# Performance work log

Hardware: AMD Instinct MI355X
Metric: run time of the kernel (lower is better)

The kernel has to match this reference:

```python
import jax, jax.numpy as jnp
import numpy as np
from jax import lax

_SQ2 = np.sqrt(2.0)
_H2 = (np.array([[1.0, 1.0], [1.0, -1.0]]) / _SQ2).astype(np.complex64)
_BN_INV = 1.0 / np.sqrt(1.0 + 1e-5)  # eval-mode BN, running_mean=0, running_var=1

# wire 0 is the most-significant bit of the 4-qubit basis index (PennyLane convention)
def _cnot_perm(c, t):
    p = np.arange(16)
    for b in range(16):
        if (b >> (3 - c)) & 1:
            p[b] = b ^ (1 << (3 - t))
    return p

# CNOT(0,1) then CNOT(1,2) then CNOT(2,3) then CNOT(3,0); psi_out = psi_in[perm]
_p01, _p12, _p23, _p30 = _cnot_perm(0, 1), _cnot_perm(1, 2), _cnot_perm(2, 3), _cnot_perm(3, 0)
_PTOT = _p01[_p12[_p23[_p30]]]
# PauliZ expectation signs: (16 basis states, 4 wires)
_ZM = np.array([[1.0 - 2.0 * ((b >> (3 - w)) & 1) for w in range(4)] for b in range(16)], np.float32)


def _make_unitaries(w0, w1):
    """w0, w1: (C,2). Circuit: H^4 -> RY(w0[0],w0[1],w0[0],w0[1]) -> RZ(w1 same pattern) -> CNOT ring."""
    ty = jnp.stack([w0[:, 0], w0[:, 1], w0[:, 0], w0[:, 1]], axis=1)  # (C,4)
    tz = jnp.stack([w1[:, 0], w1[:, 1], w1[:, 0], w1[:, 1]], axis=1)
    c, s = jnp.cos(ty / 2), jnp.sin(ty / 2)
    ry = jnp.stack([jnp.stack([c, -s], -1), jnp.stack([s, c], -1)], -2).astype(jnp.complex64)  # (C,4,2,2)
    ph = jnp.exp(-0.5j * tz.astype(jnp.complex64))  # (C,4)
    zr = jnp.zeros_like(ph)
    rz = jnp.stack([jnp.stack([ph, zr], -1), jnp.stack([zr, jnp.conj(ph)], -1)], -2)  # (C,4,2,2)
    g = rz @ ry @ jnp.asarray(_H2)  # per-wire single-qubit gate, (C,4,2,2)
    U = g[:, 0]
    for w in range(1, 4):  # kron over wires 0..3
        d = U.shape[1]
        U = jnp.einsum('cij,ckl->cikjl', U, g[:, w]).reshape(U.shape[0], d * 2, d * 2)
    return U[:, _PTOT, :]  # fold the CNOT-ring permutation into U


def _conv_bn_relu(x, w, g, b):
    y = lax.conv_general_dilated(x, w, (1, 1), ((1, 1), (1, 1)),
                                 dimension_numbers=('NCHW', 'OIHW', 'NCHW'))
    y = y * (g * _BN_INV)[None, :, None, None] + b[None, :, None, None]
    return jax.nn.relu(y)


def _bn_relu(x, g, b):
    return jax.nn.relu(x * (g * _BN_INV)[None, :, None, None] + b[None, :, None, None])


def _maxpool2(x):
    return lax.reduce_window(x, -jnp.inf, lax.max, (1, 1, 2, 2), (1, 1, 2, 2), 'VALID')


def _quantum_stage(e4, q_w0, q_w1):
    B, C, H, W = e4.shape
    xp = jnp.pad(e4, ((0, 0), (0, 0), (1, 2), (1, 2)))  # F.pad(1,2,1,2)
    # 4x4 patches, stride 1, row-major (matches torch unfold->view ordering): (B,C,H,W,16)
    patches = jnp.stack([xp[:, :, i:i + H, j:j + W] for i in range(4) for j in range(4)], axis=-1)
    nrm = jnp.sqrt(jnp.sum(patches * patches, axis=-1, keepdims=True))
    psi0 = (patches / jnp.maximum(nrm, 1e-12)).astype(jnp.complex64)  # AmplitudeEmbedding(normalize=True)
    U = _make_unitaries(q_w0, q_w1)  # (C,16,16) complex
    psi = jnp.einsum('cij,bchwj->bchwi', U, psi0)
    probs = psi.real ** 2 + psi.imag ** 2
    ev = jnp.einsum('bchwi,iq->bchwq', probs, jnp.asarray(_ZM))  # <Z_w> per wire
    return (ev.mean(-1) + 1.0) / 2.0


def setup_inputs() -> dict:
    key = jax.random.key(0)
    ks = jax.random.split(key, 18)
    conv_w = lambda k, o, i: jax.random.normal(k, (o, i, 3, 3), jnp.float32) / np.sqrt(i * 9)
    gamma = lambda k, c: jax.random.uniform(k, (c,), jnp.float32, 0.75, 1.25)
    beta = lambda k, c: 0.1 * jax.random.normal(k, (c,), jnp.float32)
    return {
        'x': jax.random.normal(ks[0], (8, 1, 256, 256), jnp.float32),
        'w1': conv_w(ks[1], 32, 1), 'g1': gamma(ks[2], 32), 'b1': beta(ks[3], 32),
        'w2': conv_w(ks[4], 64, 32), 'g2': gamma(ks[5], 64), 'b2': beta(ks[6], 64),
        'w3': conv_w(ks[7], 128, 64), 'g3': gamma(ks[8], 128), 'b3': beta(ks[9], 128),
        'w4': conv_w(ks[10], 256, 128), 'g4': gamma(ks[11], 256), 'b4': beta(ks[12], 256),
        'q_w0': 0.5 * jax.random.normal(ks[13], (256, 2), jnp.float32),
        'q_w1': 0.5 * jax.random.normal(ks[14], (256, 2), jnp.float32),
        'g5': gamma(ks[15], 256), 'b5': beta(ks[16], 256),
    }


def reference(x, w1, g1, b1, w2, g2, b2, w3, g3, b3, w4, g4, b4, q_w0, q_w1, g5, b5):
    e1 = _conv_bn_relu(x, w1, g1, b1)                 # (8,32,256,256)
    e2 = _conv_bn_relu(_maxpool2(e1), w2, g2, b2)     # (8,64,128,128)
    e3 = _conv_bn_relu(_maxpool2(e2), w3, g3, b3)     # (8,128,64,64)
    e4 = _conv_bn_relu(_maxpool2(e3), w4, g4, b4)     # (8,256,32,32)
    q = _quantum_stage(e4, q_w0, q_w1)                # (8,256,32,32)
    out4 = _bn_relu(q, g5, b5)
    return (e1, e2, e3, out4)
```

## Files before the change

### kernel.cpp

```cpp
#include <hip/hip_runtime.h>
#include <cstdint>
#include <cstddef>

#define BN_INV 0.9999950000374997f

typedef __attribute__((ext_vector_type(8))) _Float16 h8v;
typedef __attribute__((ext_vector_type(4))) float f4v;
typedef __attribute__((ext_vector_type(2))) float f2v;

__device__ __forceinline__ void fsplit(float v, ushort& h, ushort& l) {
    _Float16 hh = (_Float16)v;
    _Float16 ll = (_Float16)(v - (float)hh);
    h = __builtin_bit_cast(ushort, hh);
    l = __builtin_bit_cast(ushort, ll);
}

__device__ __forceinline__ void repack_one(
    const float* __restrict__ w, ushort* __restrict__ dst, int CIN, int i)
{
    int ocf = i / (CIN * 9);
    int r = i % (CIN * 9);
    int ic = r / 9;
    int tap = r % 9;
    int ocg = ocf >> 6, oc = ocf & 63;
    int chunk = ic >> 5, q = (ic >> 3) & 3, j = ic & 7;
    int nch = CIN >> 5;
    ushort h, l;
    fsplit(w[i], h, l);
    size_t base = (size_t)((ocg * nch + chunk) * 2) * 18432
                + (size_t)tap * 2048 + q * 512 + oc * 8 + j;
    dst[base] = h;
    dst[base + 18432] = l;
}

__global__ __launch_bounds__(256) void prep_conv1_kernel(
    const float* __restrict__ w0, const float* __restrict__ w1,
    float* __restrict__ U,
    const float* __restrict__ w2, ushort* __restrict__ wb2,
    const float* __restrict__ w3, ushort* __restrict__ wb3,
    const float* __restrict__ w4, ushort* __restrict__ wb4,
    const float* __restrict__ x, const float* __restrict__ wt,
    const float* __restrict__ g, const float* __restrict__ be,
    float* __restrict__ out, ushort* __restrict__ pooled)
{
    __shared__ float s_in[4][132];

    int blk = blockIdx.x;
    int tid = threadIdx.x;

    if (blk >= 2048) {
        if (blk >= 2424)     { repack_one(w4, wb4, 128, (blk - 2424) * 256 + tid); return; }
        if (blk >= 2136)     { repack_one(w3, wb3,  64, (blk - 2136) * 256 + tid); return; }
        if (blk >= 2064)     { repack_one(w2, wb2,  32, (blk - 2064) * 256 + tid); return; }

        int idx = (blk - 2048) * 256 + tid;
        int c = idx >> 4, r = idx & 15;
        float gr[4][2][2], gi[4][2][2];
        const float inv_sq2 = 0.70710678118654752f;
#pragma unroll
        for (int w = 0; w < 4; ++w) {
            float ty = w0[c * 2 + (w & 1)];
            float tz = w1[c * 2 + (w & 1)];
            float cy = cosf(0.5f * ty), sy = sinf(0.5f * ty);
            float cz = cosf(0.5f * tz), sz = sinf(0.5f * tz);
            float r00 = (cy - sy) * inv_sq2, r01 = (cy + sy) * inv_sq2;
            float r10 = (cy + sy) * inv_sq2, r11 = (sy - cy) * inv_sq2;
            gr[w][0][0] = cz * r00; gi[w][0][0] = -sz * r00;
            gr[w][0][1] = cz * r01; gi[w][0][1] = -sz * r01;
            gr[w][1][0] = cz * r10; gi[w][1][0] =  sz * r10;
            gr[w][1][1] = cz * r11; gi[w][1][1] =  sz * r11;
        }
        const int PTOT[16] = {0,13,3,14,6,11,5,8,12,1,15,2,10,7,9,4};
        int rp = PTOT[r];
        float* Uo = U + (size_t)c * 512 + r * 32;
#pragma unroll
        for (int cc = 0; cc < 16; ++cc) {
            float pr = 1.f, pi = 0.f;
#pragma unroll
            for (int w = 0; w < 4; ++w) {
                int ib = (rp >> (3 - w)) & 1, jb = (cc >> (3 - w)) & 1;
                float ar = gr[w][ib][jb], ai = gi[w][ib][jb];
                float nr = pr * ar - pi * ai;
                float ni = pr * ai + pi * ar;
                pr = nr; pi = ni;
            }
            Uo[cc * 2 + 0] = pr;
            Uo[cc * 2 + 1] = pi;
        }
        return;
    }

    int b = blk >> 8;
    int rest = blk & 255;
    int ty0 = (rest >> 1) * 2;
    int tx0 = (rest & 1) * 128;

    for (int i = tid; i < 520; i += 256) {
        int yy = i / 130, xx = i % 130;
        int gy = ty0 + yy - 1, gx = tx0 + xx - 1;
        float v = 0.f;
        if (gy >= 0 && gy < 256 && gx >= 0 && gx < 256)
            v = x[(size_t)b * 65536 + gy * 256 + gx];
        s_in[yy][xx] = v;
    }
    __syncthreads();

    int xx = ((tid >> 2) << 1) | (tid & 1);
    int yy = (tid >> 1) & 1;
    float t[3][3];
#pragma unroll
    for (int i = 0; i < 3; ++i)
#pragma unroll
        for (int j = 0; j < 3; ++j) t[i][j] = s_in[yy + i][xx + j];

    bool wr_pool = (tid & 3) == 0;
    ushort* op = pooled + (((size_t)b * 128 + (ty0 >> 1)) * 128 + (tx0 >> 1) + (tid >> 2)) * 64;

    size_t obase = ((size_t)b * 32) * 65536 + (size_t)(ty0 + yy) * 256 + (tx0 + xx);
#pragma unroll
    for (int k = 0; k < 4; ++k) {
        uint4 uh, ul;
#pragma unroll
        for (int j = 0; j < 8; ++j) {
            const int oc = k * 8 + j;
            float s = wt[oc*9+0] * t[0][0] + wt[oc*9+1] * t[0][1] + wt[oc*9+2] * t[0][2]
                    + wt[oc*9+3] * t[1][0] + wt[oc*9+4] * t[1][1] + wt[oc*9+5] * t[1][2]
                    + wt[oc*9+6] * t[2][0] + wt[oc*9+7] * t[2][1] + wt[oc*9+8] * t[2][2];
            s = s * (g[oc] * BN_INV) + be[oc];
            s = fmaxf(s, 0.f);
            out[obase + (size_t)oc * 65536] = s;
            float p = fmaxf(s, __shfl_xor(s, 1));
            p = fmaxf(p, __shfl_xor(p, 2));
            ushort h, l;
            fsplit(p, h, l);
            uint hw = (uint)h, lw = (uint)l;
            if (j == 0) { uh.x = hw; ul.x = lw; }
            else if (j == 1) { uh.x |= hw << 16; ul.x |= lw << 16; }
            else if (j == 2) { uh.y = hw; ul.y = lw; }
            else if (j == 3) { uh.y |= hw << 16; ul.y |= lw << 16; }
            else if (j == 4) { uh.z = hw; ul.z = lw; }
            else if (j == 5) { uh.z |= hw << 16; ul.z |= lw << 16; }
            else if (j == 6) { uh.w = hw; ul.w = lw; }
            else             { uh.w |= hw << 16; ul.w |= lw << 16; }
        }
        if (wr_pool) {
            *(uint4*)(op + 8 * k) = uh;
            *(uint4*)(op + 32 + 8 * k) = ul;
        }
    }
}

template <int CIN, int COUT, int HW, bool POOL>
__global__ __launch_bounds__(512) void conv3x3_mfma_split(
    const ushort* __restrict__ in,
    const ushort* __restrict__ wb,
    const float* __restrict__ g, const float* __restrict__ be,
    float* __restrict__ out,
    ushort* __restrict__ pooled)
{
    constexpr int NCH = CIN / 32;
    constexpr int NTX = HW / 16;
    constexpr int NT = NTX * (HW / 8);
    constexpr int NOCG = COUT / 64;
    constexpr int PS = 72;
    constexpr int BUFSZ = 180 * PS;
    constexpr int NBUF = (NCH > 1) ? 2 : 1;

    __shared__ __align__(16) ushort s_in[NBUF * BUFSZ];

    constexpr int NWG = NT * NOCG * 8;
    int bid = blockIdx.x;
    bid = (bid & 7) * (NWG >> 3) + (bid >> 3);

    int tile = bid % NT;
    int rest = bid / NT;
    int ocg = rest % NOCG;
    int b = rest / NOCG;
    int x0 = (tile % NTX) * 16;
    int y0 = (tile / NTX) * 8;

    int tid = threadIdx.x;
    int wv = tid >> 6;
    int lane = tid & 63;
    int n = lane & 15;
    int q = lane >> 4;
    int oc_half = (wv & 1) * 32;
    int sg = wv >> 1;

    int ib[2];
#pragma unroll
    for (int f = 0; f < 2; ++f)
        ib[f] = ((sg * 2 + f) * 18 + n) * PS + q * 8;
    int iwa0 = q * 512 + (oc_half + n) * 8;
    int iwa1 = q * 512 + (oc_half + 16 + n) * 8;

    const ushort* inb = in + (size_t)b * HW * HW * 2 * CIN;

    f4v acc[2][2];
#pragma unroll
    for (int a = 0; a < 2; ++a)
#pragma unroll
        for (int f = 0; f < 2; ++f) acc[a][f] = (f4v){0.f, 0.f, 0.f, 0.f};

    auto stage = [&](int ch, int bsel) {
#pragma unroll
        for (int it = 0; it < 6; ++it) {
            int i = tid + it * 512;
            if (i < 2880) {
                int pos = i >> 4;
                int r2 = i & 15;
                int comp = r2 >> 3;
                int u = r2 & 7;
                int py = pos / 18, px = pos % 18;
                int gy = y0 - 1 + py, gx = x0 - 1 + px;
                uint2 v; v.x = 0u; v.y = 0u;
                if (gy >= 0 && gy < HW && gx >= 0 && gx < HW)
                    v = *(const uint2*)(inb + ((size_t)gy * HW + gx) * (2 * CIN)
                                        + comp * CIN + ch * 32 + u * 4);
                *(uint2*)(&s_in[bsel * BUFSZ + pos * PS + comp * 32 + u * 4]) = v;
            }
        }
    };

    stage(0, 0);
    int cur = 0;
    for (int ch = 0; ch < NCH; ++ch) {
        __syncthreads();
        if (ch + 1 < NCH) stage(ch + 1, cur ^ 1);

        const ushort* wc = wb + (size_t)((ocg * NCH + ch) * 2) * 18432;
        const ushort* sb = &s_in[cur * BUFSZ];
        __builtin_amdgcn_s_setprio(1);
#pragma unroll 3
        for (int tap = 0; tap < 9; ++tap) {
            const int toff = ((tap / 3) * 18 + (tap % 3)) * PS;
            const ushort* wt_ = wc + tap * 2048;
            h8v ah0 = *(const h8v*)(wt_ + iwa0);
            h8v ah1 = *(const h8v*)(wt_ + iwa1);
            h8v al0 = *(const h8v*)(wt_ + 18432 + iwa0);
            h8v al1 = *(const h8v*)(wt_ + 18432 + iwa1);
            h8v bh[2], bl[2];
#pragma unroll
            for (int f = 0; f < 2; ++f) {
                bh[f] = *(const h8v*)(&sb[toff + ib[f]]);
                bl[f] = *(const h8v*)(&sb[toff + ib[f] + 32]);
            }
#pragma unroll
            for (int f = 0; f < 2; ++f) {
                acc[0][f] = __builtin_amdgcn_mfma_f32_16x16x32_f16(ah0, bh[f], acc[0][f], 0, 0, 0);
                acc[1][f] = __builtin_amdgcn_mfma_f32_16x16x32_f16(ah1, bh[f], acc[1][f], 0, 0, 0);
            }
#pragma unroll
            for (int f = 0; f < 2; ++f) {
                acc[0][f] = __builtin_amdgcn_mfma_f32_16x16x32_f16(ah0, bl[f], acc[0][f], 0, 0, 0);
                acc[1][f] = __builtin_amdgcn_mfma_f32_16x16x32_f16(ah1, bl[f], acc[1][f], 0, 0, 0);
            }
#pragma unroll
            for (int f = 0; f < 2; ++f) {
                acc[0][f] = __builtin_amdgcn_mfma_f32_16x16x32_f16(al0, bh[f], acc[0][f], 0, 0, 0);
                acc[1][f] = __builtin_amdgcn_mfma_f32_16x16x32_f16(al1, bh[f], acc[1][f], 0, 0, 0);
            }
        }
        __builtin_amdgcn_s_setprio(0);
        cur ^= (NBUF - 1);
    }

    float vr[2][2][4];
#pragma unroll
    for (int tf = 0; tf < 2; ++tf)
#pragma unroll
        for (int f = 0; f < 2; ++f) {
            int y = y0 + sg * 2 + f;
#pragma unroll
            for (int r = 0; r < 4; ++r) {
                int oc = ocg * 64 + oc_half + tf * 16 + q * 4 + r;
                float v = fmaxf(acc[tf][f][r] * (g[oc] * BN_INV) + be[oc], 0.f);
                vr[tf][f][r] = v;
                out[((size_t)(b * COUT + oc) * HW + y) * HW + (x0 + n)] = v;
            }
        }

    if (POOL) {
#pragma unroll
        for (int tf = 0; tf < 2; ++tf) {
            ushort h[4], l[4];
#pragma unroll
            for (int r = 0; r < 4; ++r) {
                float p = fmaxf(vr[tf][0][r], vr[tf][1][r]);
                p = fmaxf(p, __shfl_xor(p, 1));
                fsplit(p, h[r], l[r]);
            }
            if ((n & 1) == 0) {
                int pyp = (y0 >> 1) + sg;
                int pxp = (x0 + n) >> 1;
                int ocb = ocg * 64 + oc_half + tf * 16 + q * 4;
                ushort* op = pooled
                    + (((size_t)b * (HW / 2) + pyp) * (HW / 2) + pxp) * (2 * COUT);
                uint2 uh, ul;
                uh.x = (uint)h[0] | ((uint)h[1] << 16);
                uh.y = (uint)h[2] | ((uint)h[3] << 16);
                ul.x = (uint)l[0] | ((uint)l[1] << 16);
                ul.y = (uint)l[2] | ((uint)l[3] << 16);
                *(uint2*)(op + ocb) = uh;
                *(uint2*)(op + COUT + ocb) = ul;
            }
        }
    }
}

__global__ __launch_bounds__(256) void quantum_bn_relu(
    const float* __restrict__ e4,
    const float* __restrict__ U,
    const float* __restrict__ g5, const float* __restrict__ b5,
    float* __restrict__ out)
{
    int blk = blockIdx.x;
    int c = blk & 255;
    __shared__ float sp[35][36];
    __shared__ __align__(16) float sU[512];

    int tid = threadIdx.x;
    for (int i = tid; i < 35 * 36; i += 256) ((float*)sp)[i] = 0.f;
    const float4* Usrc = (const float4*)(U + (size_t)c * 512);
    if (tid < 128) ((float4*)sU)[tid] = Usrc[tid];
    float4 pv = ((const float4*)(e4 + (size_t)blk * 1024))[tid];
    __syncthreads();
    {
        int y = tid >> 3, x4 = (tid & 7) << 2;
        sp[y + 1][x4 + 1] = pv.x;
        sp[y + 1][x4 + 2] = pv.y;
        sp[y + 1][x4 + 3] = pv.z;
        sp[y + 1][x4 + 4] = pv.w;
    }
    __syncthreads();

    int y = tid >> 3, x4 = (tid & 7) << 2;
    float rows[4][8];
#pragma unroll
    for (int i = 0; i < 4; ++i) {
        float4 a = *(const float4*)&sp[y + i][x4];
        float4 bq = *(const float4*)&sp[y + i][x4 + 4];
        rows[i][0] = a.x;  rows[i][1] = a.y;  rows[i][2] = a.z;  rows[i][3] = a.w;
        rows[i][4] = bq.x; rows[i][5] = bq.y; rows[i][6] = bq.z; rows[i][7] = bq.w;
    }

    float inv2[4];
#pragma unroll
    for (int k = 0; k < 4; ++k) {
        float ss = 0.f;
#pragma unroll
        for (int i = 0; i < 4; ++i)
#pragma unroll
            for (int j = 0; j < 4; ++j) {
                float v = rows[i][k + j];
                ss += v * v;
            }
        float inv = 1.f / fmaxf(sqrtf(ss), 1e-12f);
        inv2[k] = inv * inv;
    }

    const int   RI[10] = {0, 1, 2, 4, 7, 8, 11, 13, 14, 15};
    const float ZM[10] = {1.f, .5f, .5f, .5f, -.5f, .5f, -.5f, -.5f, -.5f, -1.f};
    const float4* sU4 = (const float4*)sU;

    float s[4] = {0.f, 0.f, 0.f, 0.f};
#pragma unroll
    for (int ii = 0; ii < 10; ++ii) {
        int i = RI[ii];
        f2v p0 = {0.f, 0.f}, p1 = {0.f, 0.f}, p2 = {0.f, 0.f}, p3 = {0.f, 0.f};
#pragma unroll
        for (int jj = 0; jj < 8; ++jj) {
            float4 u = sU4[i * 8 + jj];
            f2v u01 = {u.x, u.y};
            f2v u23 = {u.z, u.w};
            const int e0 = 2 * jj, e1 = 2 * jj + 1;
            p0 += u01 * rows[e0 >> 2][0 + (e0 & 3)];
            p1 += u01 * rows[e0 >> 2][1 + (e0 & 3)];
            p2 += u01 * rows[e0 >> 2][2 + (e0 & 3)];
            p3 += u01 * rows[e0 >> 2][3 + (e0 & 3)];
            p0 += u23 * rows[e1 >> 2][0 + (e1 & 3)];
            p1 += u23 * rows[e1 >> 2][1 + (e1 & 3)];
            p2 += u23 * rows[e1 >> 2][2 + (e1 & 3)];
            p3 += u23 * rows[e1 >> 2][3 + (e1 & 3)];
        }
        float zm = ZM[ii];
        s[0] += (p0.x * p0.x + p0.y * p0.y) * zm;
        s[1] += (p1.x * p1.x + p1.y * p1.y) * zm;
        s[2] += (p2.x * p2.x + p2.y * p2.y) * zm;
        s[3] += (p3.x * p3.x + p3.y * p3.y) * zm;
    }

    float sc = g5[c] * BN_INV, bi = b5[c];
    float4 o;
    o.x = fmaxf(((s[0] * inv2[0] + 1.f) * 0.5f) * sc + bi, 0.f);
    o.y = fmaxf(((s[1] * inv2[1] + 1.f) * 0.5f) * sc + bi, 0.f);
    o.z = fmaxf(((s[2] * inv2[2] + 1.f) * 0.5f) * sc + bi, 0.f);
    o.w = fmaxf(((s[3] * inv2[3] + 1.f) * 0.5f) * sc + bi, 0.f);
    *(float4*)(out + (size_t)blk * 1024 + y * 32 + x4) = o;
}

extern "C" void kernel_launch(void* const* d_in, const int* in_sizes, int n_in,
                              void* d_out, int out_size, void* d_ws, size_t ws_size,
                              hipStream_t stream)
{
    const float* x   = (const float*)d_in[0];
    const float* w1  = (const float*)d_in[1];
    const float* g1  = (const float*)d_in[2];
    const float* b1  = (const float*)d_in[3];
    const float* w2  = (const float*)d_in[4];
    const float* g2  = (const float*)d_in[5];
    const float* b2  = (const float*)d_in[6];
    const float* w3  = (const float*)d_in[7];
    const float* g3  = (const float*)d_in[8];
    const float* b3  = (const float*)d_in[9];
    const float* w4  = (const float*)d_in[10];
    const float* g4  = (const float*)d_in[11];
    const float* b4  = (const float*)d_in[12];
    const float* qw0 = (const float*)d_in[13];
    const float* qw1 = (const float*)d_in[14];
    const float* g5  = (const float*)d_in[15];
    const float* b5  = (const float*)d_in[16];

    float* out = (float*)d_out;
    float* e1  = out;
    float* e2  = out + 16777216;
    float* e3  = out + 25165824;
    float* o4  = out + 29360128;

    float* ws = (float*)d_ws;
    float*  Uw  = ws;
    ushort* wb2 = (ushort*)(ws + 131072);
    ushort* wb3 = (ushort*)(ws + 149504);
    ushort* wb4 = (ushort*)(ws + 223232);
    ushort* pt1 = (ushort*)(ws + 518144);
    ushort* pt2 = (ushort*)(ws + 4712448);
    ushort* pt3 = (ushort*)(ws + 518144);

    prep_conv1_kernel<<<2048 + 1528, 256, 0, stream>>>(
        qw0, qw1, Uw, w2, wb2, w3, wb3, w4, wb4,
        x, w1, g1, b1, e1, pt1);

    conv3x3_mfma_split<32, 64, 128, true><<<1024, 512, 0, stream>>>(pt1, wb2, g2, b2, e2, pt2);

    conv3x3_mfma_split<64, 128, 64, true><<<512, 512, 0, stream>>>(pt2, wb3, g3, b3, e3, pt3);

    conv3x3_mfma_split<128, 256, 32, false><<<256, 512, 0, stream>>>(pt3, wb4, g4, b4, o4, nullptr);

    quantum_bn_relu<<<2048, 256, 0, stream>>>(o4, Uw, g5, b5, o4);
}
```

Measured before the change: 248.2 us.

## Retile conv1 to 4-row blocks with paired outputs; split-stage conv2 input load

The first conv kernel now processes four rows per block, so it launches half as many conv blocks. Each thread computes two adjacent x outputs as float2 vectors, writes them with paired stores, and packs the fp16 hi/lo pool values with cvt_pkrtz. For the single-chunk conv2 case, the input tile is staged in two parts: the rows needed for the first three taps are loaded first, and the remaining loads are issued before those taps run and stored to LDS after them, overlapping global latency with MFMA work. This removes the double-buffer loop for NCH==1, at the cost of an extra barrier and more code paths.

```diff
diff --git a/kernel.cpp b/kernel.cpp
--- a/kernel.cpp
+++ b/kernel.cpp
@@ -43,17 +43,17 @@
     const float* __restrict__ g, const float* __restrict__ be,
     float* __restrict__ out, ushort* __restrict__ pooled)
 {
-    __shared__ float s_in[4][132];
+    __shared__ float s_in[6][132];
 
     int blk = blockIdx.x;
     int tid = threadIdx.x;
 
-    if (blk >= 2048) {
-        if (blk >= 2424)     { repack_one(w4, wb4, 128, (blk - 2424) * 256 + tid); return; }
-        if (blk >= 2136)     { repack_one(w3, wb3,  64, (blk - 2136) * 256 + tid); return; }
-        if (blk >= 2064)     { repack_one(w2, wb2,  32, (blk - 2064) * 256 + tid); return; }
-
-        int idx = (blk - 2048) * 256 + tid;
+    if (blk >= 1024) {
+        if (blk >= 1400)     { repack_one(w4, wb4, 128, (blk - 1400) * 256 + tid); return; }
+        if (blk >= 1112)     { repack_one(w3, wb3,  64, (blk - 1112) * 256 + tid); return; }
+        if (blk >= 1040)     { repack_one(w2, wb2,  32, (blk - 1040) * 256 + tid); return; }
+
+        int idx = (blk - 1024) * 256 + tid;
         int c = idx >> 4, r = idx & 15;
         float gr[4][2][2], gi[4][2][2];
         const float inv_sq2 = 0.70710678118654752f;
@@ -90,12 +90,12 @@
         return;
     }
 
-    int b = blk >> 8;
-    int rest = blk & 255;
-    int ty0 = (rest >> 1) * 2;
+    int b = blk >> 7;
+    int rest = blk & 127;
+    int ty0 = (rest >> 1) * 4;
     int tx0 = (rest & 1) * 128;
 
-    for (int i = tid; i < 520; i += 256) {
+    for (int i = tid; i < 780; i += 256) {
         int yy = i / 130, xx = i % 130;
         int gy = ty0 + yy - 1, gx = tx0 + xx - 1;
         float v = 0.f;
@@ -105,45 +105,66 @@
     }
     __syncthreads();
 
-    int xx = ((tid >> 2) << 1) | (tid & 1);
-    int yy = (tid >> 1) & 1;
-    float t[3][3];
-#pragma unroll
-    for (int i = 0; i < 3; ++i)
-#pragma unroll
-        for (int j = 0; j < 3; ++j) t[i][j] = s_in[yy + i][xx + j];
-
-    bool wr_pool = (tid & 3) == 0;
-    ushort* op = pooled + (((size_t)b * 128 + (ty0 >> 1)) * 128 + (tx0 >> 1) + (tid >> 2)) * 64;
-
-    size_t obase = ((size_t)b * 32) * 65536 + (size_t)(ty0 + yy) * 256 + (tx0 + xx);
+    int w = tid >> 6;
+    int lane = tid & 63;
+    int xp = (w & 1) * 32 + (lane >> 1);
+    int ylo = lane & 1;
+    int y = (w >> 1) * 2 + ylo;
+    int x0s = xp * 2;
+
+    f2v t2[3][3];
+#pragma unroll
+    for (int i = 0; i < 3; ++i) {
+        f2v a = *(const f2v*)&s_in[y + i][x0s];
+        f2v bq = *(const f2v*)&s_in[y + i][x0s + 2];
+        t2[i][0] = a;
+        t2[i][1] = (f2v){a.y, bq.x};
+        t2[i][2] = bq;
+    }
+
+    bool wr_pool = (ylo == 0);
+    int pyp = (ty0 >> 1) + (w >> 1);
+    int pxp = (tx0 >> 1) + xp;
+    ushort* op = pooled + (((size_t)b * 128 + pyp) * 128 + pxp) * 64;
+    size_t obase = ((size_t)b * 32) * 65536 + (size_t)(ty0 + y) * 256 + (tx0 + x0s);
+
 #pragma unroll
     for (int k = 0; k < 4; ++k) {
-        uint4 uh, ul;
-#pragma unroll
-        for (int j = 0; j < 8; ++j) {
-            const int oc = k * 8 + j;
-            float s = wt[oc*9+0] * t[0][0] + wt[oc*9+1] * t[0][1] + wt[oc*9+2] * t[0][2]
-                    + wt[oc*9+3] * t[1][0] + wt[oc*9+4] * t[1][1] + wt[oc*9+5] * t[1][2]
-                    + wt[oc*9+6] * t[2][0] + wt[oc*9+7] * t[2][1] + wt[oc*9+8] * t[2][2];
-            s = s * (g[oc] * BN_INV) + be[oc];
-            s = fmaxf(s, 0.f);
-            out[obase + (size_t)oc * 65536] = s;
-            float p = fmaxf(s, __shfl_xor(s, 1));
-            p = fmaxf(p, __shfl_xor(p, 2));
-            ushort h, l;
-            fsplit(p, h, l);
-            uint hw = (uint)h, lw = (uint)l;
-            if (j == 0) { uh.x = hw; ul.x = lw; }
-            else if (j == 1) { uh.x |= hw << 16; ul.x |= lw << 16; }
-            else if (j == 2) { uh.y = hw; ul.y = lw; }
-            else if (j == 3) { uh.y |= hw << 16; ul.y |= lw << 16; }
-            else if (j == 4) { uh.z = hw; ul.z = lw; }
-            else if (j == 5) { uh.z |= hw << 16; ul.z |= lw << 16; }
-            else if (j == 6) { uh.w = hw; ul.w = lw; }
-            else             { uh.w |= hw << 16; ul.w |= lw << 16; }
+        uint uhw[4], ulw[4];
+#pragma unroll
+        for (int j2 = 0; j2 < 4; ++j2) {
+            const int oc0 = k * 8 + j2 * 2;
+            const int oc1 = oc0 + 1;
+            f2v s0 = {0.f, 0.f}, s1 = {0.f, 0.f};
+#pragma unroll
+            for (int i = 0; i < 3; ++i)
+#pragma unroll
+                for (int j = 0; j < 3; ++j) {
+                    s0 += wt[oc0 * 9 + i * 3 + j] * t2[i][j];
+                    s1 += wt[oc1 * 9 + i * 3 + j] * t2[i][j];
+                }
+            float gs0 = g[oc0] * BN_INV, be0 = be[oc0];
+            float gs1 = g[oc1] * BN_INV, be1 = be[oc1];
+            s0 = s0 * gs0 + (f2v){be0, be0};
+            s1 = s1 * gs1 + (f2v){be1, be1};
+            s0.x = fmaxf(s0.x, 0.f); s0.y = fmaxf(s0.y, 0.f);
+            s1.x = fmaxf(s1.x, 0.f); s1.y = fmaxf(s1.y, 0.f);
+            *(f2v*)(out + obase + (size_t)oc0 * 65536) = s0;
+            *(f2v*)(out + obase + (size_t)oc1 * 65536) = s1;
+            float p0 = fmaxf(s0.x, s0.y);
+            float p1 = fmaxf(s1.x, s1.y);
+            p0 = fmaxf(p0, __shfl_xor(p0, 1));
+            p1 = fmaxf(p1, __shfl_xor(p1, 1));
+            auto hh = __builtin_amdgcn_cvt_pkrtz(p0, p1);
+            uhw[j2] = __builtin_bit_cast(uint, hh);
+            float l0 = p0 - (float)hh.x;
+            float l1 = p1 - (float)hh.y;
+            auto ll = __builtin_amdgcn_cvt_pkrtz(l0, l1);
+            ulw[j2] = __builtin_bit_cast(uint, ll);
         }
         if (wr_pool) {
+            uint4 uh = {uhw[0], uhw[1], uhw[2], uhw[3]};
+            uint4 ul = {ulw[0], ulw[1], ulw[2], ulw[3]};
             *(uint4*)(op + 8 * k) = uh;
             *(uint4*)(op + 32 + 8 * k) = ul;
         }
@@ -202,68 +223,114 @@
 #pragma unroll
         for (int f = 0; f < 2; ++f) acc[a][f] = (f4v){0.f, 0.f, 0.f, 0.f};
 
-    auto stage = [&](int ch, int bsel) {
-#pragma unroll
-        for (int it = 0; it < 6; ++it) {
+    auto elem_addr = [&](int i, int& ldsoff, const ushort*& gsrc) {
+        int pos = i >> 4;
+        int r2 = i & 15;
+        int comp = r2 >> 3;
+        int u = r2 & 7;
+        int py = pos / 18, px = pos % 18;
+        int gy = y0 - 1 + py, gx = x0 - 1 + px;
+        ldsoff = pos * PS + comp * 32 + u * 4;
+        gsrc = (gy >= 0 && gy < HW && gx >= 0 && gx < HW)
+             ? inb + ((size_t)gy * HW + gx) * (2 * CIN) + comp * CIN + u * 4
+             : nullptr;
+    };
+
+#define TAPS(T0, T1)                                                             \
+    _Pragma("unroll")                                                            \
+    for (int tap = T0; tap < T1; ++tap) {                                        \
+        const int toff = ((tap / 3) * 18 + (tap % 3)) * PS;                      \
+        const ushort* wt_ = wc + tap * 2048;                                     \
+        h8v ah0 = *(const h8v*)(wt_ + iwa0);                                     \
+        h8v ah1 = *(const h8v*)(wt_ + iwa1);                                     \
+        h8v al0 = *(const h8v*)(wt_ + 18432 + iwa0);                             \
+        h8v al1 = *(const h8v*)(wt_ + 18432 + iwa1);                             \
+        h8v bh[2], bl[2];                                                        \
+        _Pragma("unroll")                                                        \
+        for (int f = 0; f < 2; ++f) {                                            \
+            bh[f] = *(const h8v*)(&sb[toff + ib[f]]);                            \
+            bl[f] = *(const h8v*)(&sb[toff + ib[f] + 32]);                       \
+        }                                                                        \
+        _Pragma("unroll")                                                        \
+        for (int f = 0; f < 2; ++f) {                                            \
+            acc[0][f] = __builtin_amdgcn_mfma_f32_16x16x32_f16(ah0, bh[f], acc[0][f], 0, 0, 0); \
+            acc[1][f] = __builtin_amdgcn_mfma_f32_16x16x32_f16(ah1, bh[f], acc[1][f], 0, 0, 0); \
+        }                                                                        \
+        _Pragma("unroll")                                                        \
+        for (int f = 0; f < 2; ++f) {                                            \
+            acc[0][f] = __builtin_amdgcn_mfma_f32_16x16x32_f16(ah0, bl[f], acc[0][f], 0, 0, 0); \
+            acc[1][f] = __builtin_amdgcn_mfma_f32_16x16x32_f16(ah1, bl[f], acc[1][f], 0, 0, 0); \
+        }                                                                        \
+        _Pragma("unroll")                                                        \
+        for (int f = 0; f < 2; ++f) {                                            \
+            acc[0][f] = __builtin_amdgcn_mfma_f32_16x16x32_f16(al0, bh[f], acc[0][f], 0, 0, 0); \
+            acc[1][f] = __builtin_amdgcn_mfma_f32_16x16x32_f16(al1, bh[f], acc[1][f], 0, 0, 0); \
+        }                                                                        \
+    }
+
+    if constexpr (NCH == 1) {
+#pragma unroll
+        for (int it = 0; it < 5; ++it) {
             int i = tid + it * 512;
-            if (i < 2880) {
-                int pos = i >> 4;
-                int r2 = i & 15;
-                int comp = r2 >> 3;
-                int u = r2 & 7;
-                int py = pos / 18, px = pos % 18;
-                int gy = y0 - 1 + py, gx = x0 - 1 + px;
+            if (i < 2304) {
+                int lo; const ushort* src;
+                elem_addr(i, lo, src);
                 uint2 v; v.x = 0u; v.y = 0u;
-                if (gy >= 0 && gy < HW && gx >= 0 && gx < HW)
-                    v = *(const uint2*)(inb + ((size_t)gy * HW + gx) * (2 * CIN)
-                                        + comp * CIN + ch * 32 + u * 4);
-                *(uint2*)(&s_in[bsel * BUFSZ + pos * PS + comp * 32 + u * 4]) = v;
-            }
-        }
-    };
-
-    stage(0, 0);
-    int cur = 0;
-    for (int ch = 0; ch < NCH; ++ch) {
+                if (src) v = *(const uint2*)src;
+                *(uint2*)(&s_in[lo]) = v;
+            }
+        }
+        int lo0, lo1 = 0; const ushort* src0; const ushort* src1 = nullptr;
+        elem_addr(2304 + tid, lo0, src0);
+        bool has1 = tid < 64;
+        if (has1) elem_addr(2816 + tid, lo1, src1);
+        uint2 v0; v0.x = 0u; v0.y = 0u;
+        uint2 v1; v1.x = 0u; v1.y = 0u;
+        if (src0) v0 = *(const uint2*)src0;
+        if (src1) v1 = *(const uint2*)src1;
         __syncthreads();
-        if (ch + 1 < NCH) stage(ch + 1, cur ^ 1);
-
-        const ushort* wc = wb + (size_t)((ocg * NCH + ch) * 2) * 18432;
-        const ushort* sb = &s_in[cur * BUFSZ];
+
+        const ushort* wc = wb + (size_t)(ocg * 2) * 18432;
+        const ushort* sb = &s_in[0];
         __builtin_amdgcn_s_setprio(1);
-#pragma unroll 3
-        for (int tap = 0; tap < 9; ++tap) {
-            const int toff = ((tap / 3) * 18 + (tap % 3)) * PS;
-            const ushort* wt_ = wc + tap * 2048;
-            h8v ah0 = *(const h8v*)(wt_ + iwa0);
-            h8v ah1 = *(const h8v*)(wt_ + iwa1);
-            h8v al0 = *(const h8v*)(wt_ + 18432 + iwa0);
-            h8v al1 = *(const h8v*)(wt_ + 18432 + iwa1);
-            h8v bh[2], bl[2];
-#pragma unroll
-            for (int f = 0; f < 2; ++f) {
-                bh[f] = *(const h8v*)(&sb[toff + ib[f]]);
-                bl[f] = *(const h8v*)(&sb[toff + ib[f] + 32]);
-            }
-#pragma unroll
-            for (int f = 0; f < 2; ++f) {
-                acc[0][f] = __builtin_amdgcn_mfma_f32_16x16x32_f16(ah0, bh[f], acc[0][f], 0, 0, 0);
-                acc[1][f] = __builtin_amdgcn_mfma_f32_16x16x32_f16(ah1, bh[f], acc[1][f], 0, 0, 0);
-            }
-#pragma unroll
-            for (int f = 0; f < 2; ++f) {
-                acc[0][f] = __builtin_amdgcn_mfma_f32_16x16x32_f16(ah0, bl[f], acc[0][f], 0, 0, 0);
-                acc[1][f] = __builtin_amdgcn_mfma_f32_16x16x32_f16(ah1, bl[f], acc[1][f], 0, 0, 0);
-            }
-#pragma unroll
-            for (int f = 0; f < 2; ++f) {
-                acc[0][f] = __builtin_amdgcn_mfma_f32_16x16x32_f16(al0, bh[f], acc[0][f], 0, 0, 0);
-                acc[1][f] = __builtin_amdgcn_mfma_f32_16x16x32_f16(al1, bh[f], acc[1][f], 0, 0, 0);
-            }
-        }
+        TAPS(0, 3)
         __builtin_amdgcn_s_setprio(0);
-        cur ^= (NBUF - 1);
-    }
+        *(uint2*)(&s_in[lo0]) = v0;
+        if (has1) *(uint2*)(&s_in[lo1]) = v1;
+        __syncthreads();
+        __builtin_amdgcn_s_setprio(1);
+        TAPS(3, 9)
+        __builtin_amdgcn_s_setprio(0);
+    } else {
+        auto stage = [&](int ch, int bsel) {
+#pragma unroll
+            for (int it = 0; it < 6; ++it) {
+                int i = tid + it * 512;
+                if (i < 2880) {
+                    int lo; const ushort* src;
+                    elem_addr(i, lo, src);
+                    uint2 v; v.x = 0u; v.y = 0u;
+                    if (src) v = *(const uint2*)(src + (size_t)ch * 32);
+                    *(uint2*)(&s_in[bsel * BUFSZ + lo]) = v;
+                }
+            }
+        };
+
+        stage(0, 0);
+        int cur = 0;
+        for (int ch = 0; ch < NCH; ++ch) {
+            __syncthreads();
+            if (ch + 1 < NCH) stage(ch + 1, cur ^ 1);
+
+            const ushort* wc = wb + (size_t)((ocg * NCH + ch) * 2) * 18432;
+            const ushort* sb = &s_in[cur * BUFSZ];
+            __builtin_amdgcn_s_setprio(1);
+            TAPS(0, 9)
+            __builtin_amdgcn_s_setprio(0);
+            cur ^= 1;
+        }
+    }
+#undef TAPS
 
     float vr[2][2][4];
 #pragma unroll
@@ -436,7 +503,7 @@
     ushort* pt2 = (ushort*)(ws + 4712448);
     ushort* pt3 = (ushort*)(ws + 518144);
 
-    prep_conv1_kernel<<<2048 + 1528, 256, 0, stream>>>(
+    prep_conv1_kernel<<<2552, 256, 0, stream>>>(
         qw0, qw1, Uw, w2, wb2, w3, wb3, w4, wb4,
         x, w1, g1, b1, e1, pt1);
 
```

Result: faster. 242.7 us (-2.2%).
